# Optimization experiments

Hardware: AMD Instinct MI355X
Metric: run time of the kernel (lower is better)

The kernel has to match this reference:

```python
import jax, jax.numpy as jnp
import numpy as np

W_PROFILE, W_PLANFORM, W_MEAN = 0.5, 0.3, 0.2
CELL_SIZE = 10.0
EPS = 1e-08


def _kernels():
    sobel_x = np.array([[-1, 0, 1], [-2, 0, 2], [-1, 0, 1]], np.float32) / 8.0
    sobel_y = np.array([[-1, -2, -1], [0, 0, 0], [1, 2, 1]], np.float32) / 8.0
    k_xx = np.array([[1, -2, 1], [1, -2, 1], [1, -2, 1]], np.float32) / 3.0
    k_yy = np.array([[1, 1, 1], [-2, -2, -2], [1, 1, 1]], np.float32) / 3.0
    k_xy = np.array([[-1, 0, 1], [0, 0, 0], [1, 0, -1]], np.float32) / 4.0
    # stack into one [5,1,3,3] OIHW kernel -> single fused conv for all 5 stencils
    return jnp.asarray(np.stack([sobel_x, sobel_y, k_xx, k_xy, k_yy])[:, None])

_K = _kernels()


def _curvatures(dem):
    # dem: [B,1,H,W] -> derivatives p,q,r,s,t each [B,1,H,W]
    d = jax.lax.conv_general_dilated(dem, _K, window_strides=(1, 1), padding='SAME',
                                     dimension_numbers=('NCHW', 'OIHW', 'NCHW'))
    p = d[:, 0:1] / CELL_SIZE
    q = d[:, 1:2] / CELL_SIZE
    r = d[:, 2:3] / CELL_SIZE ** 2
    s = d[:, 3:4] / CELL_SIZE ** 2
    t = d[:, 4:5] / CELL_SIZE ** 2
    p2, q2, pq = p * p, q * q, p * q
    denom1 = p2 + q2
    denom2 = (1 + denom1) ** 1.5
    profile = (r * p2 + 2 * s * pq + t * q2) / (denom1 * jnp.sqrt(1 + denom1) + EPS)
    planform = (r * q2 - 2 * s * pq + t * p2) / (denom1 ** 1.5 + EPS)
    mean = ((1 + q2) * r - 2 * pq * s + (1 + p2) * t) / (2 * denom2 + EPS)
    flat = denom1 < EPS
    profile = jnp.where(flat, 0.0, profile)
    planform = jnp.where(flat, 0.0, planform)
    return profile, planform, mean


def setup_inputs() -> dict:
    key = jax.random.key(0)
    k1, k2 = jax.random.split(key)
    shape = (16, 1, 1024, 1024)
    return {
        'pred': jax.random.normal(k1, shape, dtype=jnp.float32),
        'target': jax.random.normal(k2, shape, dtype=jnp.float32),
    }


def reference(pred, target):
    pp, pl, pm = _curvatures(pred)
    tp, tl, tm = _curvatures(target)
    loss_profile = jnp.mean(jnp.abs(pp - tp))
    loss_planform = jnp.mean(jnp.abs(pl - tl))
    loss_mean = jnp.mean(jnp.abs(pm - tm))
    return W_PROFILE * loss_profile + W_PLANFORM * loss_planform + W_MEAN * loss_mean
```

## Files before the change

### kernel.cpp

```cpp
#include <hip/hip_runtime.h>
#include <math.h>

constexpr int IMG_B = 16;
constexpr int IMG_H = 1024;
constexpr int IMG_W = 1024;
constexpr int ROWS_PER_THREAD = 8;
constexpr int BLOCK = 256;
constexpr int BX_TILES = IMG_W / BLOCK;
constexpr int BY_TILES = IMG_H / ROWS_PER_THREAD;
constexpr int NBLOCKS  = IMG_B * BY_TILES * BX_TILES;
constexpr float EPS = 1e-8f;

__device__ __forceinline__ void curv3(
    float a00, float a01, float a02,
    float a10, float a11, float a12,
    float a20, float a21, float a22,
    float& prof, float& plan, float& mean)
{
    const float t1 = a02 - a00;
    const float t2 = a22 - a20;
    const float t3 = a12 - a10;
    const float gx = (t1 + t2) + 2.0f * t3;
    const float t4 = a20 - a00;
    const float t5 = a22 - a02;
    const float t6 = a21 - a01;
    const float gy = (t4 + t5) + 2.0f * t6;
    const float r0 = a00 + a01 + a02;
    const float r1 = a10 + a11 + a12;
    const float r2 = a20 + a21 + a22;
    const float tot = (r0 + r2) + r1;
    const float c1 = (a01 + a21) + a11;
    const float rxx = tot - 3.0f * c1;
    const float tyy = tot - 3.0f * r1;
    const float sxy = t1 - t2;

    const float p = gx * (1.0f / 80.0f);
    const float q = gy * (1.0f / 80.0f);
    const float r = rxx * (1.0f / 300.0f);
    const float s = sxy * (1.0f / 400.0f);
    const float t = tyy * (1.0f / 300.0f);

    const float p2 = p * p, q2 = q * q, pq = p * q;
    const float d1 = p2 + q2;
    const float od = 1.0f + d1;
    const float sq_od = __builtin_amdgcn_sqrtf(od);
    const float sq_d  = __builtin_amdgcn_sqrtf(d1);
    const float s2pq = 2.0f * s * pq;
    const float nprof = (r * p2 + s2pq) + t * q2;
    const float nplan = (r * q2 - s2pq) + t * p2;
    const float nmean = ((1.0f + q2) * r - 2.0f * pq * s) + (1.0f + p2) * t;

    prof = nprof * __builtin_amdgcn_rcpf(d1 * sq_od + EPS);
    plan = nplan * __builtin_amdgcn_rcpf(d1 * sq_d + EPS);
    mean = nmean * __builtin_amdgcn_rcpf(2.0f * od * sq_od + EPS);
    if (d1 < EPS) { prof = 0.0f; plan = 0.0f; }
}

__global__ __launch_bounds__(BLOCK) void curv_loss_main(
    const float* __restrict__ pred, const float* __restrict__ targ,
    float* __restrict__ blocksums)
{
    const int tid = threadIdx.x;
    int b = blockIdx.x;
    const int bx  = b & (BX_TILES - 1);
    const int by  = (b >> 2) & (BY_TILES - 1);
    const int img = b >> 9;
    const int x  = bx * BLOCK + tid;
    const int y0 = by * ROWS_PER_THREAD;
    const size_t base = (size_t)img * (size_t)(IMG_H * IMG_W);
    const float* __restrict__ P = pred + base;
    const float* __restrict__ T = targ + base;
    const bool xm_ok = (x > 0);
    const bool xp_ok = (x < IMG_W - 1);

    auto loadrow = [&](const float* __restrict__ A, int y,
                       float& c0, float& c1, float& c2) {
        if ((unsigned)y < (unsigned)IMG_H) {
            const int o = y * IMG_W + x;
            c1 = A[o];
            c0 = xm_ok ? A[o - 1] : 0.0f;
            c2 = xp_ok ? A[o + 1] : 0.0f;
        } else {
            c0 = 0.0f; c1 = 0.0f; c2 = 0.0f;
        }
    };

    float pa0, pa1, pa2, pb0, pb1, pb2, pc0, pc1, pc2;
    float ta0, ta1, ta2, tb0, tb1, tb2, tc0, tc1, tc2;
    loadrow(P, y0 - 1, pa0, pa1, pa2);
    loadrow(T, y0 - 1, ta0, ta1, ta2);
    loadrow(P, y0,     pb0, pb1, pb2);
    loadrow(T, y0,     tb0, tb1, tb2);

    float acc = 0.0f;
#pragma unroll
    for (int i = 0; i < ROWS_PER_THREAD; ++i) {
        loadrow(P, y0 + i + 1, pc0, pc1, pc2);
        loadrow(T, y0 + i + 1, tc0, tc1, tc2);
        float pp, pl, pm, qp, ql, qm;
        curv3(pa0, pa1, pa2, pb0, pb1, pb2, pc0, pc1, pc2, pp, pl, pm);
        curv3(ta0, ta1, ta2, tb0, tb1, tb2, tc0, tc1, tc2, qp, ql, qm);
        acc += 0.5f * fabsf(pp - qp) + 0.3f * fabsf(pl - ql) + 0.2f * fabsf(pm - qm);
        pa0 = pb0; pa1 = pb1; pa2 = pb2;
        pb0 = pc0; pb1 = pc1; pb2 = pc2;
        ta0 = tb0; ta1 = tb1; ta2 = tb2;
        tb0 = tc0; tb1 = tc1; tb2 = tc2;
    }

    for (int off = 32; off > 0; off >>= 1) acc += __shfl_down(acc, off, 64);
    __shared__ float ws[BLOCK / 64];
    const int lane = tid & 63, wid = tid >> 6;
    if (lane == 0) ws[wid] = acc;
    __syncthreads();
    if (tid == 0)
        blocksums[blockIdx.x] = (ws[0] + ws[1]) + (ws[2] + ws[3]);
}

__global__ __launch_bounds__(BLOCK) void curv_loss_final(
    const float* __restrict__ blocksums, float* __restrict__ out)
{
    const int tid = threadIdx.x;
    float v = 0.0f;
    for (int i = tid; i < NBLOCKS; i += BLOCK) v += blocksums[i];
    for (int off = 32; off > 0; off >>= 1) v += __shfl_down(v, off, 64);
    __shared__ float ws[BLOCK / 64];
    const int lane = tid & 63, wid = tid >> 6;
    if (lane == 0) ws[wid] = v;
    __syncthreads();
    if (tid == 0) {
        const float tot = (ws[0] + ws[1]) + (ws[2] + ws[3]);
        out[0] = tot * (1.0f / (float)(IMG_B * IMG_H * IMG_W));
    }
}

extern "C" void kernel_launch(void* const* d_in, const int* in_sizes, int n_in,
                              void* d_out, int out_size, void* d_ws, size_t ws_size,
                              hipStream_t stream)
{
    const float* pred = (const float*)d_in[0];
    const float* targ = (const float*)d_in[1];
    float* out = (float*)d_out;
    float* blocksums = (float*)d_ws;

    curv_loss_main<<<NBLOCKS, BLOCK, 0, stream>>>(pred, targ, blocksums);
    curv_loss_final<<<1, BLOCK, 0, stream>>>(blocksums, out);
}
```

Measured before the change: 171.0 us.

## Process four columns per thread with float4 loads and separable row prefactors

```diff
diff --git a/kernel.cpp b/kernel.cpp
--- a/kernel.cpp
+++ b/kernel.cpp
@@ -1,58 +1,78 @@
 #include <hip/hip_runtime.h>
 #include <math.h>
+
 
 constexpr int IMG_B = 16;
 constexpr int IMG_H = 1024;
 constexpr int IMG_W = 1024;
-constexpr int ROWS_PER_THREAD = 8;
+constexpr int ROWS  = 8;
 constexpr int BLOCK = 256;
-constexpr int BX_TILES = IMG_W / BLOCK;
-constexpr int BY_TILES = IMG_H / ROWS_PER_THREAD;
-constexpr int NBLOCKS  = IMG_B * BY_TILES * BX_TILES;
+constexpr int TILES_Y = IMG_H / ROWS;
+constexpr int NBLOCKS = IMG_B * TILES_Y;
 constexpr float EPS = 1e-8f;
 
-__device__ __forceinline__ void curv3(
-    float a00, float a01, float a02,
-    float a10, float a11, float a12,
-    float a20, float a21, float a22,
-    float& prof, float& plan, float& mean)
+constexpr float A2  = 1.0f / 6400.0f;
+constexpr float Bc  = 1.0f / 300.0f;
+constexpr float C2  = 1.0f / 200.0f;
+
+struct Row { float hx[4]; float hs[4]; float rs[4]; };
+
+__device__ __forceinline__ void prep_row(const float* __restrict__ A, int y,
+                                         bool okl, bool okr, Row& o)
 {
-    const float t1 = a02 - a00;
-    const float t2 = a22 - a20;
-    const float t3 = a12 - a10;
-    const float gx = (t1 + t2) + 2.0f * t3;
-    const float t4 = a20 - a00;
-    const float t5 = a22 - a02;
-    const float t6 = a21 - a01;
-    const float gy = (t4 + t5) + 2.0f * t6;
-    const float r0 = a00 + a01 + a02;
-    const float r1 = a10 + a11 + a12;
-    const float r2 = a20 + a21 + a22;
-    const float tot = (r0 + r2) + r1;
-    const float c1 = (a01 + a21) + a11;
-    const float rxx = tot - 3.0f * c1;
-    const float tyy = tot - 3.0f * r1;
-    const float sxy = t1 - t2;
+    if ((unsigned)y < (unsigned)IMG_H) {
+        const size_t off = (size_t)y << 10;
+        const float4 v = *reinterpret_cast<const float4*>(A + off);
+        const float l = okl ? A[off - 1] : 0.0f;
+        const float r = okr ? A[off + 4] : 0.0f;
+        const float w[6] = {l, v.x, v.y, v.z, v.w, r};
+#pragma unroll
+        for (int j = 0; j < 4; ++j) {
+            const float e = w[j] + w[j + 2];
+            o.hx[j] = w[j + 2] - w[j];
+            o.hs[j] = fmaf(2.0f, w[j + 1], e);
+            o.rs[j] = e + w[j + 1];
+        }
+    } else {
+#pragma unroll
+        for (int j = 0; j < 4; ++j) { o.hx[j] = 0.f; o.hs[j] = 0.f; o.rs[j] = 0.f; }
+    }
+}
 
-    const float p = gx * (1.0f / 80.0f);
-    const float q = gy * (1.0f / 80.0f);
-    const float r = rxx * (1.0f / 300.0f);
-    const float s = sxy * (1.0f / 400.0f);
-    const float t = tyy * (1.0f / 300.0f);
+__device__ __forceinline__ void curv(const Row& a, const Row& b, const Row& c, int j,
+                                     float& prof, float& plan, float& mean)
+{
+    const float gx  = fmaf(2.0f, b.hx[j], a.hx[j] + c.hx[j]);
+    const float gy  = c.hs[j] - a.hs[j];
+    const float tot = (a.rs[j] + c.rs[j]) + b.rs[j];
+    const float H   = (a.hs[j] + c.hs[j]) + b.hs[j];
+    const float c1  = H - tot;
+    const float rxx = fmaf(-3.0f, c1, tot);
+    const float tyy = fmaf(-3.0f, b.rs[j], tot);
+    const float sxy = a.hx[j] - c.hx[j];
 
-    const float p2 = p * p, q2 = q * q, pq = p * q;
-    const float d1 = p2 + q2;
-    const float od = 1.0f + d1;
+    const float gx2 = gx * gx, gy2 = gy * gy, gxgy = gx * gy;
+    const float g2  = gx2 + gy2;
+    const float d1  = A2 * g2;
+    const float od  = 1.0f + d1;
+
     const float sq_od = __builtin_amdgcn_sqrtf(od);
-    const float sq_d  = __builtin_amdgcn_sqrtf(d1);
-    const float s2pq = 2.0f * s * pq;
-    const float nprof = (r * p2 + s2pq) + t * q2;
-    const float nplan = (r * q2 - s2pq) + t * p2;
-    const float nmean = ((1.0f + q2) * r - 2.0f * pq * s) + (1.0f + p2) * t;
+    const float sq_d1 = __builtin_amdgcn_sqrtf(d1);
 
-    prof = nprof * __builtin_amdgcn_rcpf(d1 * sq_od + EPS);
-    plan = nplan * __builtin_amdgcn_rcpf(d1 * sq_d + EPS);
-    mean = nmean * __builtin_amdgcn_rcpf(2.0f * od * sq_od + EPS);
+    const float h1   = fmaf(tyy, gy2, rxx * gx2);
+    const float h3   = fmaf(tyy, gx2, rxx * gy2);
+    const float h2c  = C2 * (sxy * gxgy);
+    const float nprof = A2 * fmaf(Bc, h1, h2c);
+    const float nplan = A2 * fmaf(Bc, h3, -h2c);
+    const float mnum  = fmaf(Bc, rxx + tyy, nplan);
+
+    const float den_p = fmaf(d1, sq_od, EPS);
+    const float den_l = fmaf(d1, sq_d1, EPS);
+    const float den_m = fmaf(od + od, sq_od, EPS);
+
+    prof = nprof * __builtin_amdgcn_rcpf(den_p);
+    plan = nplan * __builtin_amdgcn_rcpf(den_l);
+    mean = mnum  * __builtin_amdgcn_rcpf(den_m);
     if (d1 < EPS) { prof = 0.0f; plan = 0.0f; }
 }
 
@@ -61,59 +81,47 @@
     float* __restrict__ blocksums)
 {
     const int tid = threadIdx.x;
-    int b = blockIdx.x;
-    const int bx  = b & (BX_TILES - 1);
-    const int by  = (b >> 2) & (BY_TILES - 1);
-    const int img = b >> 9;
-    const int x  = bx * BLOCK + tid;
-    const int y0 = by * ROWS_PER_THREAD;
-    const size_t base = (size_t)img * (size_t)(IMG_H * IMG_W);
+    const int b   = blockIdx.x;
+    const int img = b >> 7;
+    const int ty  = b & (TILES_Y - 1);
+    const int y0  = ty * ROWS;
+    const size_t base = (size_t)img * (size_t)(IMG_H * IMG_W) + 4 * tid;
     const float* __restrict__ P = pred + base;
     const float* __restrict__ T = targ + base;
-    const bool xm_ok = (x > 0);
-    const bool xp_ok = (x < IMG_W - 1);
+    const bool okl = (tid > 0);
+    const bool okr = (tid < BLOCK - 1);
 
-    auto loadrow = [&](const float* __restrict__ A, int y,
-                       float& c0, float& c1, float& c2) {
-        if ((unsigned)y < (unsigned)IMG_H) {
-            const int o = y * IMG_W + x;
-            c1 = A[o];
-            c0 = xm_ok ? A[o - 1] : 0.0f;
-            c2 = xp_ok ? A[o + 1] : 0.0f;
-        } else {
-            c0 = 0.0f; c1 = 0.0f; c2 = 0.0f;
-        }
-    };
-
-    float pa0, pa1, pa2, pb0, pb1, pb2, pc0, pc1, pc2;
-    float ta0, ta1, ta2, tb0, tb1, tb2, tc0, tc1, tc2;
-    loadrow(P, y0 - 1, pa0, pa1, pa2);
-    loadrow(T, y0 - 1, ta0, ta1, ta2);
-    loadrow(P, y0,     pb0, pb1, pb2);
-    loadrow(T, y0,     tb0, tb1, tb2);
+    Row pr[3], tr[3];
+    prep_row(P, y0 - 1, okl, okr, pr[0]);
+    prep_row(T, y0 - 1, okl, okr, tr[0]);
+    prep_row(P, y0,     okl, okr, pr[1]);
+    prep_row(T, y0,     okl, okr, tr[1]);
 
     float acc = 0.0f;
 #pragma unroll
-    for (int i = 0; i < ROWS_PER_THREAD; ++i) {
-        loadrow(P, y0 + i + 1, pc0, pc1, pc2);
-        loadrow(T, y0 + i + 1, tc0, tc1, tc2);
-        float pp, pl, pm, qp, ql, qm;
-        curv3(pa0, pa1, pa2, pb0, pb1, pb2, pc0, pc1, pc2, pp, pl, pm);
-        curv3(ta0, ta1, ta2, tb0, tb1, tb2, tc0, tc1, tc2, qp, ql, qm);
-        acc += 0.5f * fabsf(pp - qp) + 0.3f * fabsf(pl - ql) + 0.2f * fabsf(pm - qm);
-        pa0 = pb0; pa1 = pb1; pa2 = pb2;
-        pb0 = pc0; pb1 = pc1; pb2 = pc2;
-        ta0 = tb0; ta1 = tb1; ta2 = tb2;
-        tb0 = tc0; tb1 = tc1; tb2 = tc2;
+    for (int i = 0; i < ROWS; ++i) {
+        const int ia = i % 3, ib = (i + 1) % 3, ic = (i + 2) % 3;
+        prep_row(P, y0 + i + 1, okl, okr, pr[ic]);
+        prep_row(T, y0 + i + 1, okl, okr, tr[ic]);
+#pragma unroll
+        for (int j = 0; j < 4; ++j) {
+            float pp, pl, pm, qp, ql, qm;
+            curv(pr[ia], pr[ib], pr[ic], j, pp, pl, pm);
+            curv(tr[ia], tr[ib], tr[ic], j, qp, ql, qm);
+            acc = fmaf(0.5f, fabsf(pp - qp), acc);
+            acc = fmaf(0.3f, fabsf(pl - ql), acc);
+            acc = fmaf(0.2f, fabsf(pm - qm), acc);
+        }
     }
 
+#pragma unroll
     for (int off = 32; off > 0; off >>= 1) acc += __shfl_down(acc, off, 64);
     __shared__ float ws[BLOCK / 64];
     const int lane = tid & 63, wid = tid >> 6;
     if (lane == 0) ws[wid] = acc;
     __syncthreads();
     if (tid == 0)
-        blocksums[blockIdx.x] = (ws[0] + ws[1]) + (ws[2] + ws[3]);
+        blocksums[b] = (ws[0] + ws[1]) + (ws[2] + ws[3]);
 }
 
 __global__ __launch_bounds__(BLOCK) void curv_loss_final(
@@ -121,7 +129,9 @@
 {
     const int tid = threadIdx.x;
     float v = 0.0f;
-    for (int i = tid; i < NBLOCKS; i += BLOCK) v += blocksums[i];
+#pragma unroll
+    for (int i = 0; i < NBLOCKS / BLOCK; ++i) v += blocksums[i * BLOCK + tid];
+#pragma unroll
     for (int off = 32; off > 0; off >>= 1) v += __shfl_down(v, off, 64);
     __shared__ float ws[BLOCK / 64];
     const int lane = tid & 63, wid = tid >> 6;
```

Result: slower. 185.6 us (+8.6%).
